# Kernel optimization log

Measured on AMD Instinct MI355X. Metric: run time of the kernel, lower is better.

The kernel has to match this reference:

```python
import jax, jax.numpy as jnp
import numpy as np

L = 512      # x_len (also per-segment memory length)
B = 4        # batch
D = 512      # d_model
H = 8        # num_head
DH = 64      # d_head
MEM = 3      # mem_num (number of cached memory segments)
TOTAL = (MEM + 1) * L
SCALE = 1.0 / (DH ** 0.5)
LN_EPS = 1e-5


def setup_inputs() -> dict:
    key = jax.random.key(0)
    ks = jax.random.split(key, 12)
    f = lambda k, s: jax.random.normal(k, s, dtype=jnp.float32)
    x = f(ks[0], (L, B, D))
    memory = f(ks[1], (MEM, L, B, D))
    pos_emb = f(ks[2], (TOTAL, B, D))
    pos_bias_u = f(ks[3], (H, DH)) * 0.02
    pos_bias_v = f(ks[4], (H, DH)) * 0.02
    # segment gate: random 0/1, but current-input segment (last) always on
    ib = (jax.random.uniform(ks[5], (L, B, MEM + 1)) < 0.7).astype(jnp.float32)
    indice_bool = ib.at[:, :, MEM].set(1.0)
    # causal mask over concatenated [memory ; x] keys: mask future input positions
    qi = jnp.arange(L)[:, None]
    kj = jnp.arange(TOTAL)[None, :]
    mask = jnp.broadcast_to((kj > (MEM * L + qi))[:, :, None], (L, TOTAL, B))
    W_q = f(ks[6], (D, H * DH)) * 0.02
    W_kv = f(ks[7], (D, 2 * H * DH)) * 0.02
    W_rel = f(ks[8], (D, H * DH)) * 0.02
    W_o = f(ks[9], (H * DH, D)) * 0.02
    ln_g = jnp.ones((D,), jnp.float32)
    ln_b = jnp.zeros((D,), jnp.float32)
    return dict(x=x, memory=memory, pos_emb=pos_emb, pos_bias_u=pos_bias_u,
                pos_bias_v=pos_bias_v, mask=mask, indice_bool=indice_bool,
                W_q=W_q, W_kv=W_kv, W_rel=W_rel, W_o=W_o, ln_g=ln_g, ln_b=ln_b)


def _rel_shift(bd):
    # bd: [i, k, j, b, n]; torch _rel_shift flattens (k,j) and does the pad/view trick
    i, k, j, b, n = bd.shape
    xf = bd.reshape(i, k * j, b, n)
    zp = jnp.zeros((i, 1, b, n), bd.dtype)
    xp = jnp.concatenate([zp, xf], axis=1)            # [i, k*j+1, b, n]
    xp = xp.reshape(k * j + 1, i, b, n)               # raw memory reinterpretation
    return xp[1:].reshape(i, k, j, b, n)


def reference(x, memory, pos_emb, pos_bias_u, pos_bias_v, mask, indice_bool,
              W_q, W_kv, W_rel, W_o, ln_g, ln_b):
    Lq, Bz, Dm = x.shape
    mem_flat = memory.reshape(MEM * Lq, Bz, Dm)
    c = jnp.concatenate([mem_flat, x], axis=0)        # [TOTAL, B, D]
    kv = c @ W_kv                                     # [TOTAL, B, 2*H*DH]
    k_, v_ = jnp.split(kv, 2, axis=-1)
    pk = k_.reshape(MEM + 1, Lq, Bz, H, DH)
    pv = v_.reshape(MEM + 1, Lq, Bz, H, DH)
    rel = (pos_emb @ W_rel).reshape(MEM + 1, Lq, Bz, H, DH)
    q = (x @ W_q).reshape(Lq, Bz, H, DH)
    qu = q + pos_bias_u
    qv = q + pos_bias_v
    # gate[i,k,1,b,1] == indice_bool[i,b,k]; equals einsum('ibnd,ibk->kibnd') pre-mul
    gate = jnp.transpose(indice_bool, (0, 2, 1))[:, :, None, :, None]
    AC = jnp.einsum('ibnd,kjbnd->ikjbn', qu, pk) * gate   # [i,k,j,b,n]
    BD = jnp.einsum('ibnd,kjbnd->ikjbn', qv, rel) * gate
    BD = _rel_shift(BD)
    score = (AC + BD) * SCALE
    score = score.reshape(Lq, TOTAL, Bz, H)
    score = jnp.where(mask[:, :, :, None], -jnp.inf, score)
    prob = jax.nn.softmax(score, axis=1)
    attn_matrix = prob.mean(axis=(2, 3))              # [i, TOTAL]
    prob5 = prob.reshape(Lq, MEM + 1, Lq, Bz, H)
    vec = jnp.einsum('ikjbn,kjbnd->ibnd', prob5, pv).reshape(Lq, Bz, H * DH)
    attn_out = vec @ W_o
    y = x + attn_out
    mu = y.mean(-1, keepdims=True)
    var = jnp.mean(jnp.square(y - mu), axis=-1, keepdims=True)
    output = (y - mu) / jnp.sqrt(var + LN_EPS) * ln_g + ln_b
    return (output, attn_matrix)
```

## Files before the change

### kernel.cpp

```cpp
#include <hip/hip_runtime.h>
#include <hip/hip_bf16.h>
#include <math.h>

typedef __bf16 bhalf8 __attribute__((ext_vector_type(8)));
typedef __bf16 bhalf4 __attribute__((ext_vector_type(4)));
typedef float  f32x4  __attribute__((ext_vector_type(4)));

#define MFMA16(a, b, c) __builtin_amdgcn_mfma_f32_16x16x32_bf16(a, b, c, 0, 0, 0)

__global__ __launch_bounds__(256) void transcast_all(
    const float* __restrict__ Wq, const float* __restrict__ Wkv,
    const float* __restrict__ Wrel, const float* __restrict__ Wo,
    __bf16* __restrict__ Wt)
{
  const int k  = blockIdx.x * 64 + (threadIdx.x & 63);
  const int ng = blockIdx.y * 4 + (threadIdx.x >> 6);
  const float* src; int nn, Ns;
  if (ng < 512)       { src = Wq;   nn = ng;        Ns = 512; }
  else if (ng < 1536) { src = Wkv;  nn = ng - 512;  Ns = 1024; }
  else if (ng < 2048) { src = Wrel; nn = ng - 1536; Ns = 512; }
  else                { src = Wo;   nn = ng - 2048; Ns = 512; }
  Wt[(size_t)ng * 512 + k] = (__bf16)src[(size_t)k * Ns + nn];
}

template <int OUT_MODE, int A_F32>
__global__ __launch_bounds__(256) void gemm_bf16(
    const void* __restrict__ A0v, const void* __restrict__ A1v, int split,
    const __bf16* __restrict__ Bt, void* __restrict__ C, int M, int N, int K,
    const float* __restrict__ pbu, const float* __restrict__ pbv,
    __bf16* __restrict__ qup, __bf16* __restrict__ qvp)
{
  __shared__ __bf16 a_lds[128][40];
  __shared__ __bf16 b_lds[128][40];
  const int m0 = blockIdx.x * 128;
  const int n0 = blockIdx.y * 128;
  const int tid = threadIdx.x;
  const int w = tid >> 6, l = tid & 63;
  const int wn = (w >> 1) * 64, wm = (w & 1) * 64;
  const int li = l & 15, lq = l >> 4;
  const int lk = lq << 3;

  const int srow0 = tid >> 2, srow1 = (tid >> 2) + 64;
  const int skc = (tid & 3) << 3;
  const float* arowf[2];
  const __bf16* arowh[2];
  if (A_F32) {
    const float* A0 = (const float*)A0v;
    const float* A1 = (const float*)A1v;
    const int r0 = m0 + srow0, r1 = m0 + srow1;
    arowf[0] = r0 < split ? A0 + (size_t)r0 * K : A1 + (size_t)(r0 - split) * K;
    arowf[1] = r1 < split ? A0 + (size_t)r1 * K : A1 + (size_t)(r1 - split) * K;
  } else {
    arowh[0] = (const __bf16*)A0v + (size_t)(m0 + srow0) * K;
    arowh[1] = (const __bf16*)A0v + (size_t)(m0 + srow1) * K;
  }

  f32x4 acc[4][4] = {};

  for (int k0 = 0; k0 < K; k0 += 32) {
    __syncthreads();
#pragma unroll
    for (int c = 0; c < 2; ++c) {
      const int row = c ? srow1 : srow0;
      if (A_F32) {
        float4 f0 = *(const float4*)(arowf[c] + k0 + skc);
        float4 f1 = *(const float4*)(arowf[c] + k0 + skc + 4);
        bhalf8 h;
        h[0] = (__bf16)f0.x; h[1] = (__bf16)f0.y; h[2] = (__bf16)f0.z; h[3] = (__bf16)f0.w;
        h[4] = (__bf16)f1.x; h[5] = (__bf16)f1.y; h[6] = (__bf16)f1.z; h[7] = (__bf16)f1.w;
        *(bhalf8*)&a_lds[row][skc] = h;
      } else {
        *(bhalf8*)&a_lds[row][skc] = *(const bhalf8*)(arowh[c] + k0 + skc);
      }
      *(bhalf8*)&b_lds[row][skc] = *(const bhalf8*)(Bt + (size_t)(n0 + row) * K + k0 + skc);
    }
    __syncthreads();
    bhalf8 af[4], bf_[4];
#pragma unroll
    for (int s = 0; s < 4; ++s) {
      af[s]  = *(const bhalf8*)&b_lds[wn + s * 16 + li][lk];
      bf_[s] = *(const bhalf8*)&a_lds[wm + s * 16 + li][lk];
    }
#pragma unroll
    for (int ns = 0; ns < 4; ++ns)
#pragma unroll
      for (int ms = 0; ms < 4; ++ms)
        acc[ns][ms] = MFMA16(af[ns], bf_[ms], acc[ns][ms]);
  }

  const int lr = lq << 2;
#pragma unroll
  for (int ms = 0; ms < 4; ++ms) {
    const int m = m0 + wm + ms * 16 + li;
#pragma unroll
    for (int ns = 0; ns < 4; ++ns) {
      const int n = n0 + wn + ns * 16 + lr;
      if (OUT_MODE == 1) {
        *(f32x4*)((float*)C + (size_t)m * N + n) = acc[ns][ms];
      } else if (OUT_MODE == 0) {
        bhalf4 pk;
#pragma unroll
        for (int r = 0; r < 4; ++r) pk[r] = (__bf16)acc[ns][ms][r];
        *(bhalf4*)((__bf16*)C + (size_t)m * N + n) = pk;
      } else {
        const int i = m >> 2, bb = m & 3, hd = n >> 6;
        float4 u4 = *(const float4*)(pbu + n);
        float4 v4 = *(const float4*)(pbv + n);
        const size_t off = (((size_t)bb * 8 + hd) * 512 + i) * 64 + (n & 63);
        bhalf4 pu, pv;
        pu[0] = (__bf16)((acc[ns][ms][0] + u4.x) * 0.125f);
        pu[1] = (__bf16)((acc[ns][ms][1] + u4.y) * 0.125f);
        pu[2] = (__bf16)((acc[ns][ms][2] + u4.z) * 0.125f);
        pu[3] = (__bf16)((acc[ns][ms][3] + u4.w) * 0.125f);
        pv[0] = (__bf16)((acc[ns][ms][0] + v4.x) * 0.125f);
        pv[1] = (__bf16)((acc[ns][ms][1] + v4.y) * 0.125f);
        pv[2] = (__bf16)((acc[ns][ms][2] + v4.z) * 0.125f);
        pv[3] = (__bf16)((acc[ns][ms][3] + v4.w) * 0.125f);
        *(bhalf4*)(qup + off) = pu;
        *(bhalf4*)(qvp + off) = pv;
      }
    }
  }
}

__global__ __launch_bounds__(256) void vtrans(const __bf16* __restrict__ kvb,
                                              __bf16* __restrict__ vtb)
{
  __shared__ __bf16 T2[64][72];
  const int t0 = blockIdx.x * 64;
  const int p = blockIdx.y;
  const int b = p >> 3, n = p & 7;
  const int tid = threadIdx.x;
#pragma unroll
  for (int c = 0; c < 2; ++c) {
    const int e = c * 256 + tid;
    const int tl = e >> 3, d8 = (e & 7) << 3;
    bhalf8 v8 = *(const bhalf8*)(kvb + ((size_t)(t0 + tl) * 4 + b) * 1024 + 512 + n * 64 + d8);
#pragma unroll
    for (int j = 0; j < 8; ++j) T2[d8 + j][tl] = v8[j];
  }
  __syncthreads();
#pragma unroll
  for (int c = 0; c < 2; ++c) {
    const int e = c * 256 + tid;
    const int d = e >> 3, t8 = (e & 7) << 3;
    bhalf8 v = *(const bhalf8*)&T2[d][t8];
    *(bhalf8*)(vtb + ((size_t)p * 64 + d) * 2048 + t0 + t8) = v;
  }
}

__global__ __launch_bounds__(512, 4) void attn_v4(
    const __bf16* __restrict__ qup, const __bf16* __restrict__ qvp,
    const __bf16* __restrict__ kvb, const __bf16* __restrict__ relb,
    const __bf16* __restrict__ vtb, const float* __restrict__ indice,
    float* __restrict__ po, float* __restrict__ mlh,
    __bf16* __restrict__ pb, float* __restrict__ ms)
{
  __shared__ __align__(16) __bf16 P_l[32][136];
  __shared__ __align__(16) __bf16 bdl[160][34];
  __shared__ float red0[8][33];
  __shared__ float red1[8][33];

  const int bid = blockIdx.x;
  const int wrk = ((bid & 7) << 7) | (bid >> 3);
  const int plane = wrk >> 5;
  const int i0 = ((wrk >> 1) & 15) << 5;
  const int half = wrk & 1;
  const int b = plane >> 3, n = plane & 7;
  const int tid = threadIdx.x;
  const int w = tid >> 6;
  const int l = tid & 63;
  const int li = l & 15;
  const int lq = l >> 4;

  const __bf16* kbase = kvb + (size_t)b * 1024 + n * 64;
  const __bf16* rbase = relb + (size_t)b * 512 + n * 64;
  const __bf16* vbase = vtb + (size_t)plane * 131072;

  bhalf8 qu[2][2], qv[2][2];
  float g[2][4];
#pragma unroll
  for (int it = 0; it < 2; ++it) {
    const int i = i0 + it * 16 + li;
    const float* gp = indice + ((size_t)i * 4 + b) * 4;
    g[it][0] = gp[0]; g[it][1] = gp[1]; g[it][2] = gp[2]; g[it][3] = gp[3];
    const __bf16* qp = qup + ((size_t)plane * 512 + i) * 64;
    const __bf16* qq = qvp + ((size_t)plane * 512 + i) * 64;
    qu[it][0] = *(const bhalf8*)(qp + lq * 8);
    qu[it][1] = *(const bhalf8*)(qp + 32 + lq * 8);
    qv[it][0] = *(const bhalf8*)(qq + lq * 8);
    qv[it][1] = *(const bhalf8*)(qq + 32 + lq * 8);
  }

  float m0 = -1e30f, m1 = -1e30f, l0 = 0.f, l1 = 0.f;
  f32x4 oacc = {0.f, 0.f, 0.f, 0.f};
  const int dgw = w >> 1, itw = w & 1;
  const int nt = ((1536 + i0 + 31) >> 7) + 1;
  const int t_start = half ? 8 : 0;
  const int t_end   = half ? nt : 8;

  for (int tile = t_start; tile < t_end; ++tile) {
    const int tb = tile << 7;
    const int rb = tb + 480 - i0;

#pragma unroll
    for (int ri = 0; ri < 2; ++ri) {
      const int rs = w + ri * 8;
      if (ri == 0 || rs < 10) {
        int row = rb + rs * 16 + li;
        row = row > 2047 ? 2047 : row;
        const __bf16* rp = rbase + (size_t)row * 2048;
        bhalf8 a0 = *(const bhalf8*)(rp + lq * 8);
        bhalf8 a1 = *(const bhalf8*)(rp + 32 + lq * 8);
#pragma unroll
        for (int it = 0; it < 2; ++it) {
          f32x4 c = {0.f, 0.f, 0.f, 0.f};
          c = MFMA16(a0, qv[it][0], c);
          c = MFMA16(a1, qv[it][1], c);
#pragma unroll
          for (int r = 0; r < 4; ++r) {
            const int rowl = rs * 16 + lq * 4 + r;
            int rk = (rb + rowl) >> 9; rk = rk > 3 ? 3 : rk;
            bdl[rowl][it * 16 + li] = (__bf16)(c[r] * g[it][rk]);
          }
        }
      }
    }
    f32x4 s[2];
    {
      const __bf16* kp = kbase + (size_t)(tb + w * 16 + li) * 4096;
      bhalf8 a0 = *(const bhalf8*)(kp + lq * 8);
      bhalf8 a1 = *(const bhalf8*)(kp + 32 + lq * 8);
#pragma unroll
      for (int it = 0; it < 2; ++it) {
        f32x4 c = {0.f, 0.f, 0.f, 0.f};
        c = MFMA16(a0, qu[it][0], c);
        c = MFMA16(a1, qu[it][1], c);
        s[it] = c;
      }
    }
    __syncthreads();

    float sv[2][4];
    float tmax[2] = {-1e30f, -1e30f};
#pragma unroll
    for (int it = 0; it < 2; ++it) {
      const int i = i0 + it * 16 + li;
#pragma unroll
      for (int r = 0; r < 4; ++r) {
        const int tl = w * 16 + lq * 4 + r;
        const int t = tb + tl;
        float sc = -1e30f;
        if (t <= 1536 + i) {
          const float bdv = (float)bdl[tl + 31 - it * 16 - li][it * 16 + li];
          sc = s[it][r] * g[it][t >> 9] + bdv;
        }
        sv[it][r] = sc;
        tmax[it] = fmaxf(tmax[it], sc);
      }
    }
    tmax[0] = fmaxf(tmax[0], __shfl_xor(tmax[0], 16));
    tmax[0] = fmaxf(tmax[0], __shfl_xor(tmax[0], 32));
    tmax[1] = fmaxf(tmax[1], __shfl_xor(tmax[1], 16));
    tmax[1] = fmaxf(tmax[1], __shfl_xor(tmax[1], 32));
    if (l < 16) { red0[w][li] = tmax[0]; red0[w][16 + li] = tmax[1]; }
    __syncthreads();

    float mn[2], scl[2];
#pragma unroll
    for (int it = 0; it < 2; ++it) {
      const int ic = it * 16 + li;
      float mt = red0[0][ic];
#pragma unroll
      for (int ww = 1; ww < 8; ++ww) mt = fmaxf(mt, red0[ww][ic]);
      const float mo = it ? m1 : m0;
      mn[it] = fmaxf(mo, mt);
      scl[it] = __expf(mo - mn[it]);
    }
    if (w == 0 && l < 16) {
      float* msp = ms + ((size_t)plane * 16 + tile) * 512 + i0;
      msp[li] = mn[0];
      msp[16 + li] = mn[1];
    }
    float ps[2] = {0.f, 0.f};
#pragma unroll
    for (int it = 0; it < 2; ++it) {
      bhalf4 pk;
#pragma unroll
      for (int r = 0; r < 4; ++r) {
        const float p = __expf(sv[it][r] - mn[it]);
        ps[it] += p;
        pk[r] = (__bf16)p;
      }
      *(bhalf4*)&P_l[it * 16 + li][w * 16 + lq * 4] = pk;
    }
    ps[0] += __shfl_xor(ps[0], 16); ps[0] += __shfl_xor(ps[0], 32);
    ps[1] += __shfl_xor(ps[1], 16); ps[1] += __shfl_xor(ps[1], 32);
    if (l < 16) { red1[w][li] = ps[0]; red1[w][16 + li] = ps[1]; }
    __syncthreads();

    {
      const int iloc = tid >> 4, tq = tid & 15;
      bhalf8 pv8 = *(const bhalf8*)&P_l[iloc][tq * 8];
      *(bhalf8*)(pb + ((size_t)plane * 512 + i0 + iloc) * 2048 + tb + tq * 8) = pv8;
    }

    {
      float ls0 = 0.f, ls1 = 0.f;
#pragma unroll
      for (int ww = 0; ww < 8; ++ww) { ls0 += red1[ww][li]; ls1 += red1[ww][16 + li]; }
      l0 = l0 * scl[0] + ls0; m0 = mn[0];
      l1 = l1 * scl[1] + ls1; m1 = mn[1];
    }
    oacc *= scl[itw];
    {
      const __bf16* vp = vbase + (size_t)(dgw * 16 + li) * 2048 + tb;
#pragma unroll
      for (int kt = 0; kt < 4; ++kt) {
        bhalf8 af = *(const bhalf8*)(vp + kt * 32 + lq * 8);
        bhalf8 bf_ = *(const bhalf8*)&P_l[itw * 16 + li][kt * 32 + lq * 8];
        oacc = MFMA16(af, bf_, oacc);
      }
    }
  }

  __syncthreads();
  float* obuf = (float*)&P_l[0][0];
  if (w == 0 && l < 16) {
    float* mp0 = mlh + ((size_t)half * 16384 + plane * 512 + i0 + li) * 2;
    mp0[0] = m0; mp0[1] = l0;
    float* mp1 = mlh + ((size_t)half * 16384 + plane * 512 + i0 + 16 + li) * 2;
    mp1[0] = m1; mp1[1] = l1;
  }
#pragma unroll
  for (int r = 0; r < 4; ++r)
    obuf[(itw * 16 + li) * 68 + dgw * 16 + lq * 4 + r] = oacc[r];
  __syncthreads();
  {
    const int iloc = tid >> 4, dq = tid & 15;
    f32x4 o = *(f32x4*)&obuf[iloc * 68 + dq * 4];
    *(f32x4*)(po + ((size_t)half * 16384 + plane * 512 + i0 + iloc) * 64 + dq * 4) = o;
  }
}

__global__ __launch_bounds__(256) void attn_merge(
    const float* __restrict__ po, const float* __restrict__ mlh,
    __bf16* __restrict__ vecb, float* __restrict__ ml)
{
  const int row = blockIdx.x * 16 + (threadIdx.x >> 4);
  const int dq = threadIdx.x & 15;
  const float2 a = *(const float2*)(mlh + (size_t)row * 2);
  const float2 bm = *(const float2*)(mlh + ((size_t)16384 + row) * 2);
  const float mf = fmaxf(a.x, bm.x);
  const float ea = __expf(a.x - mf), eb = __expf(bm.x - mf);
  const float lf = a.y * ea + bm.y * eb;
  f32x4 oa = *(const f32x4*)(po + (size_t)row * 64 + dq * 4);
  f32x4 ob = *(const f32x4*)(po + ((size_t)16384 + row) * 64 + dq * 4);
  const float inv = 1.f / lf;
  bhalf4 ov;
#pragma unroll
  for (int r = 0; r < 4; ++r) ov[r] = (__bf16)((oa[r] * ea + ob[r] * eb) * inv);
  const int plane = row >> 9, i = row & 511, b = plane >> 3, n = plane & 7;
  *(bhalf4*)(vecb + ((size_t)i * 4 + b) * 512 + n * 64 + dq * 4) = ov;
  if (dq == 0) { ml[(size_t)row * 2] = mf; ml[(size_t)row * 2 + 1] = lf; }
}

__global__ __launch_bounds__(256) void am_final(
    const __bf16* __restrict__ pb, const float* __restrict__ ms,
    const float* __restrict__ ml, float* __restrict__ am)
{
  const int i = blockIdx.x;
  const int tid = threadIdx.x;
  const int t0 = tid << 3;
  const int tile = t0 >> 7;
  const bool valid = tile <= ((1536 + (i | 31)) >> 7);
  f32x4 a0 = {0.f, 0.f, 0.f, 0.f}, a1 = {0.f, 0.f, 0.f, 0.f};
#pragma unroll 4
  for (int p = 0; p < 32; ++p) {
    const float2 mlv = *(const float2*)(ml + ((size_t)p * 512 + i) * 2);
    float wgt = 0.f;
    if (valid)
      wgt = __expf(ms[((size_t)p * 16 + tile) * 512 + i] - mlv.x) / mlv.y;
    bhalf8 v = *(const bhalf8*)(pb + ((size_t)p * 512 + i) * 2048 + t0);
    a0[0] += wgt * (float)v[0];
    a0[1] += wgt * (float)v[1];
    a0[2] += wgt * (float)v[2];
    a0[3] += wgt * (float)v[3];
    a1[0] += wgt * (float)v[4];
    a1[1] += wgt * (float)v[5];
    a1[2] += wgt * (float)v[6];
    a1[3] += wgt * (float)v[7];
  }
  const float sc = 1.f / 32.f;
  *(f32x4*)(am + (size_t)i * 2048 + t0)     = a0 * sc;
  *(f32x4*)(am + (size_t)i * 2048 + t0 + 4) = a1 * sc;
}

__global__ __launch_bounds__(256) void ln_f32(
    const float* __restrict__ x, const float* __restrict__ ao,
    const float* __restrict__ g, const float* __restrict__ bb,
    float* __restrict__ out)
{
  const int row = blockIdx.x;
  const int tid = threadIdx.x;
  const size_t base = (size_t)row * 512;
  const float y0 = x[base + tid] + ao[base + tid];
  const float y1 = x[base + 256 + tid] + ao[base + 256 + tid];
  float s  = y0 + y1;
  float ss = y0 * y0 + y1 * y1;
#pragma unroll
  for (int off = 32; off > 0; off >>= 1) {
    s  += __shfl_xor(s, off);
    ss += __shfl_xor(ss, off);
  }
  __shared__ float sred[4], ssred[4], stat[2];
  const int w = tid >> 6;
  if ((tid & 63) == 0) { sred[w] = s; ssred[w] = ss; }
  __syncthreads();
  if (tid == 0) {
    const float S  = sred[0] + sred[1] + sred[2] + sred[3];
    const float SS = ssred[0] + ssred[1] + ssred[2] + ssred[3];
    const float mu = S * (1.f / 512.f);
    const float var = SS * (1.f / 512.f) - mu * mu;
    stat[0] = mu;
    stat[1] = rsqrtf(var + 1e-5f);
  }
  __syncthreads();
  const float mu = stat[0], rs = stat[1];
  out[base + tid]       = (y0 - mu) * rs * g[tid] + bb[tid];
  out[base + 256 + tid] = (y1 - mu) * rs * g[256 + tid] + bb[256 + tid];
}

extern "C" void kernel_launch(void* const* d_in, const int* in_sizes, int n_in,
                              void* d_out, int out_size, void* d_ws, size_t ws_size,
                              hipStream_t stream)
{
  (void)in_sizes; (void)n_in; (void)out_size; (void)ws_size;
  const float* x      = (const float*)d_in[0];
  const float* memory = (const float*)d_in[1];
  const float* pos    = (const float*)d_in[2];
  const float* pbu    = (const float*)d_in[3];
  const float* pbv    = (const float*)d_in[4];
  const float* indice = (const float*)d_in[6];
  const float* W_q    = (const float*)d_in[7];
  const float* W_kv   = (const float*)d_in[8];
  const float* W_rel  = (const float*)d_in[9];
  const float* W_o    = (const float*)d_in[10];
  const float* ln_g   = (const float*)d_in[11];
  const float* ln_b   = (const float*)d_in[12];

  float* out = (float*)d_out;
  float* am  = out + 1048576;

  __bf16* ws    = (__bf16*)d_ws;
  __bf16* vtb   = ws;
  float*  po    = (float*)(ws + 4194304);
  float*  aof   = po;
  __bf16* kvb   = ws + 8388608;
  __bf16* relb  = ws + 16777216;
  __bf16* qup   = ws + 20971520;
  __bf16* qvp   = ws + 22020096;
  __bf16* vecb  = ws + 23068672;
  __bf16* wt    = ws + 24117248;
  __bf16* wqt   = wt;
  __bf16* wkvt  = wt + 512 * 512;
  __bf16* wrelt = wt + 1536 * 512;
  __bf16* wot   = wt + 2048 * 512;
  float*  ml    = (float*)(ws + 25427968);
  float*  ms    = (float*)(ws + 25493504);
  __bf16* pbuf  = ws + 26017792;
  float*  mlh   = (float*)(ws + 59572224);

  transcast_all<<<dim3(8, 640), 256, 0, stream>>>(W_q, W_kv, W_rel, W_o, wt);

  gemm_bf16<2, 1><<<dim3(16, 4), 256, 0, stream>>>(x, x, 2048, wqt, (void*)qup,
                                                   2048, 512, 512, pbu, pbv, qup, qvp);
  gemm_bf16<0, 1><<<dim3(64, 8), 256, 0, stream>>>(memory, x, 6144, wkvt, kvb,
                                                   8192, 1024, 512,
                                                   nullptr, nullptr, nullptr, nullptr);
  gemm_bf16<0, 1><<<dim3(64, 4), 256, 0, stream>>>(pos, pos, 8192, wrelt, relb,
                                                   8192, 512, 512,
                                                   nullptr, nullptr, nullptr, nullptr);

  vtrans<<<dim3(32, 32), 256, 0, stream>>>(kvb, vtb);

  attn_v4<<<1024, 512, 0, stream>>>(qup, qvp, kvb, relb, vtb, indice,
                                    po, mlh, pbuf, ms);
  attn_merge<<<1024, 256, 0, stream>>>(po, mlh, vecb, ml);

  am_final<<<512, 256, 0, stream>>>(pbuf, ms, ml, am);

  gemm_bf16<1, 0><<<dim3(16, 4), 256, 0, stream>>>(vecb, vecb, 2048, wot, aof,
                                                   2048, 512, 512,
                                                   nullptr, nullptr, nullptr, nullptr);
  ln_f32<<<2048, 256, 0, stream>>>(x, aof, ln_g, ln_b, out);
}
```

Baseline: 305.1 us.

## Restructure attention to per-wave independent softmax with in-block merge

Rewrites the attention kernel so each wave owns a 16-query by 32-key slice and keeps its own running max and sum, removing the block-wide reductions and most of the __syncthreads calls inside the tile loop. The two key halves are no longer split across blocks; four partial softmax states are merged in shared memory at the end, which drops the separate merge kernel and its global round-trip. The per-slice max is now stored at 32-key granularity and am_final is adjusted to read it. In exchange there are half as many blocks, each wave issues more V MFMAs and redundant rel loads, and per-wave maxima are coarser.

```diff
diff --git a/kernel.cpp b/kernel.cpp
--- a/kernel.cpp
+++ b/kernel.cpp
@@ -149,220 +149,168 @@
   }
 }
 
-__global__ __launch_bounds__(512, 4) void attn_v4(
+__global__ __launch_bounds__(512, 4) void attn_v5(
     const __bf16* __restrict__ qup, const __bf16* __restrict__ qvp,
     const __bf16* __restrict__ kvb, const __bf16* __restrict__ relb,
     const __bf16* __restrict__ vtb, const float* __restrict__ indice,
-    float* __restrict__ po, float* __restrict__ mlh,
+    __bf16* __restrict__ vecb, float* __restrict__ ml,
     __bf16* __restrict__ pb, float* __restrict__ ms)
 {
-  __shared__ __align__(16) __bf16 P_l[32][136];
-  __shared__ __align__(16) __bf16 bdl[160][34];
-  __shared__ float red0[8][33];
-  __shared__ float red1[8][33];
+  __shared__ __align__(16) char smem_raw[36864];
+  __shared__ float mlw[8][16][2];
+  float*  bdw = (float*)smem_raw;
+  __bf16* pw  = (__bf16*)(smem_raw + 27648);
+  float*  obuf = (float*)smem_raw;
 
   const int bid = blockIdx.x;
-  const int wrk = ((bid & 7) << 7) | (bid >> 3);
-  const int plane = wrk >> 5;
-  const int i0 = ((wrk >> 1) & 15) << 5;
-  const int half = wrk & 1;
+  const int wrk = ((bid & 7) << 6) | (bid >> 3);
+  const int plane = wrk >> 4;
+  const int i0 = (wrk & 15) << 5;
   const int b = plane >> 3, n = plane & 7;
   const int tid = threadIdx.x;
-  const int w = tid >> 6;
-  const int l = tid & 63;
-  const int li = l & 15;
-  const int lq = l >> 4;
-
-  const __bf16* kbase = kvb + (size_t)b * 1024 + n * 64;
-  const __bf16* rbase = relb + (size_t)b * 512 + n * 64;
+  const int w = tid >> 6, l = tid & 63;
+  const int li = l & 15, lq = l >> 4;
+  const int it = w & 1, ts = w >> 1;
+  const int i = i0 + it * 16 + li;
+  const int base_r = (2 * ts + 1 - it) << 4;
+
+  float*  bdww = bdw + w * (48 * 18);
+  __bf16* pww  = pw + w * (16 * 36);
+
+  const __bf16* qp = qup + ((size_t)plane * 512 + i) * 64;
+  const __bf16* qq = qvp + ((size_t)plane * 512 + i) * 64;
+  bhalf8 qu0 = *(const bhalf8*)(qp + lq * 8);
+  bhalf8 qu1 = *(const bhalf8*)(qp + 32 + lq * 8);
+  bhalf8 qv0 = *(const bhalf8*)(qq + lq * 8);
+  bhalf8 qv1 = *(const bhalf8*)(qq + 32 + lq * 8);
+  const float* gp = indice + ((size_t)i * 4 + b) * 4;
+  const float g0 = gp[0], g1 = gp[1], g2 = gp[2], g3 = gp[3];
+
   const __bf16* vbase = vtb + (size_t)plane * 131072;
 
-  bhalf8 qu[2][2], qv[2][2];
-  float g[2][4];
-#pragma unroll
-  for (int it = 0; it < 2; ++it) {
-    const int i = i0 + it * 16 + li;
-    const float* gp = indice + ((size_t)i * 4 + b) * 4;
-    g[it][0] = gp[0]; g[it][1] = gp[1]; g[it][2] = gp[2]; g[it][3] = gp[3];
-    const __bf16* qp = qup + ((size_t)plane * 512 + i) * 64;
-    const __bf16* qq = qvp + ((size_t)plane * 512 + i) * 64;
-    qu[it][0] = *(const bhalf8*)(qp + lq * 8);
-    qu[it][1] = *(const bhalf8*)(qp + 32 + lq * 8);
-    qv[it][0] = *(const bhalf8*)(qq + lq * 8);
-    qv[it][1] = *(const bhalf8*)(qq + 32 + lq * 8);
-  }
-
-  float m0 = -1e30f, m1 = -1e30f, l0 = 0.f, l1 = 0.f;
-  f32x4 oacc = {0.f, 0.f, 0.f, 0.f};
-  const int dgw = w >> 1, itw = w & 1;
+  float m_run = -1e30f, l_run = 0.f;
+  f32x4 oacc[4] = {};
   const int nt = ((1536 + i0 + 31) >> 7) + 1;
-  const int t_start = half ? 8 : 0;
-  const int t_end   = half ? nt : 8;
-
-  for (int tile = t_start; tile < t_end; ++tile) {
+
+  for (int tile = 0; tile < nt; ++tile) {
     const int tb = tile << 7;
-    const int rb = tb + 480 - i0;
-
-#pragma unroll
-    for (int ri = 0; ri < 2; ++ri) {
-      const int rs = w + ri * 8;
-      if (ri == 0 || rs < 10) {
-        int row = rb + rs * 16 + li;
-        row = row > 2047 ? 2047 : row;
-        const __bf16* rp = rbase + (size_t)row * 2048;
-        bhalf8 a0 = *(const bhalf8*)(rp + lq * 8);
-        bhalf8 a1 = *(const bhalf8*)(rp + 32 + lq * 8);
-#pragma unroll
-        for (int it = 0; it < 2; ++it) {
-          f32x4 c = {0.f, 0.f, 0.f, 0.f};
-          c = MFMA16(a0, qv[it][0], c);
-          c = MFMA16(a1, qv[it][1], c);
-#pragma unroll
-          for (int r = 0; r < 4; ++r) {
-            const int rowl = rs * 16 + lq * 4 + r;
-            int rk = (rb + rowl) >> 9; rk = rk > 3 ? 3 : rk;
-            bdl[rowl][it * 16 + li] = (__bf16)(c[r] * g[it][rk]);
-          }
+    const int wbase = tb + 480 - i0 + base_r;
+
+#pragma unroll
+    for (int rs = 0; rs < 3; ++rs) {
+      int grow = wbase + rs * 16 + li;
+      grow = grow > 2047 ? 2047 : grow;
+      const __bf16* rp = relb + ((size_t)grow * 4 + b) * 512 + n * 64;
+      bhalf8 a0 = *(const bhalf8*)(rp + lq * 8);
+      bhalf8 a1 = *(const bhalf8*)(rp + 32 + lq * 8);
+      f32x4 c = {0.f, 0.f, 0.f, 0.f};
+      c = MFMA16(a0, qv0, c);
+      c = MFMA16(a1, qv1, c);
+#pragma unroll
+      for (int r = 0; r < 4; ++r) {
+        const int rl = rs * 16 + lq * 4 + r;
+        int rk = (wbase + rl) >> 9; rk = rk > 3 ? 3 : rk;
+        const float gk = rk == 0 ? g0 : (rk == 1 ? g1 : (rk == 2 ? g2 : g3));
+        bdww[rl * 18 + li] = c[r] * gk;
+      }
+    }
+    f32x4 s[2];
+#pragma unroll
+    for (int sl = 0; sl < 2; ++sl) {
+      const __bf16* kp = kvb + ((size_t)(tb + ts * 32 + sl * 16 + li) * 4 + b) * 1024 + n * 64;
+      f32x4 c = {0.f, 0.f, 0.f, 0.f};
+      c = MFMA16(*(const bhalf8*)(kp + lq * 8), qu0, c);
+      c = MFMA16(*(const bhalf8*)(kp + 32 + lq * 8), qu1, c);
+      s[sl] = c;
+    }
+    float sc[2][4];
+    float tmax = -1e30f;
+#pragma unroll
+    for (int sl = 0; sl < 2; ++sl) {
+#pragma unroll
+      for (int r = 0; r < 4; ++r) {
+        const int tloc = ts * 32 + sl * 16 + lq * 4 + r;
+        const int t = tb + tloc;
+        float v = -1e30f;
+        if (t <= 1536 + i) {
+          const int tk = t >> 9;
+          const float gk = tk == 0 ? g0 : (tk == 1 ? g1 : (tk == 2 ? g2 : g3));
+          v = s[sl][r] * gk + bdww[(sl * 16 + lq * 4 + r + 15 - li) * 18 + li];
         }
+        sc[sl][r] = v;
+        tmax = fmaxf(tmax, v);
       }
     }
-    f32x4 s[2];
-    {
-      const __bf16* kp = kbase + (size_t)(tb + w * 16 + li) * 4096;
-      bhalf8 a0 = *(const bhalf8*)(kp + lq * 8);
-      bhalf8 a1 = *(const bhalf8*)(kp + 32 + lq * 8);
-#pragma unroll
-      for (int it = 0; it < 2; ++it) {
-        f32x4 c = {0.f, 0.f, 0.f, 0.f};
-        c = MFMA16(a0, qu[it][0], c);
-        c = MFMA16(a1, qu[it][1], c);
-        s[it] = c;
+    tmax = fmaxf(tmax, __shfl_xor(tmax, 16));
+    tmax = fmaxf(tmax, __shfl_xor(tmax, 32));
+    const float mnew = fmaxf(m_run, tmax);
+    const float scl = __expf(m_run - mnew);
+    float psum = 0.f;
+    bhalf4 pk[2];
+#pragma unroll
+    for (int sl = 0; sl < 2; ++sl) {
+#pragma unroll
+      for (int r = 0; r < 4; ++r) {
+        const float p = __expf(sc[sl][r] - mnew);
+        psum += p;
+        pk[sl][r] = (__bf16)p;
       }
     }
-    __syncthreads();
-
-    float sv[2][4];
-    float tmax[2] = {-1e30f, -1e30f};
-#pragma unroll
-    for (int it = 0; it < 2; ++it) {
-      const int i = i0 + it * 16 + li;
-#pragma unroll
-      for (int r = 0; r < 4; ++r) {
-        const int tl = w * 16 + lq * 4 + r;
-        const int t = tb + tl;
-        float sc = -1e30f;
-        if (t <= 1536 + i) {
-          const float bdv = (float)bdl[tl + 31 - it * 16 - li][it * 16 + li];
-          sc = s[it][r] * g[it][t >> 9] + bdv;
-        }
-        sv[it][r] = sc;
-        tmax[it] = fmaxf(tmax[it], sc);
-      }
-    }
-    tmax[0] = fmaxf(tmax[0], __shfl_xor(tmax[0], 16));
-    tmax[0] = fmaxf(tmax[0], __shfl_xor(tmax[0], 32));
-    tmax[1] = fmaxf(tmax[1], __shfl_xor(tmax[1], 16));
-    tmax[1] = fmaxf(tmax[1], __shfl_xor(tmax[1], 32));
-    if (l < 16) { red0[w][li] = tmax[0]; red0[w][16 + li] = tmax[1]; }
-    __syncthreads();
-
-    float mn[2], scl[2];
-#pragma unroll
-    for (int it = 0; it < 2; ++it) {
-      const int ic = it * 16 + li;
-      float mt = red0[0][ic];
-#pragma unroll
-      for (int ww = 1; ww < 8; ++ww) mt = fmaxf(mt, red0[ww][ic]);
-      const float mo = it ? m1 : m0;
-      mn[it] = fmaxf(mo, mt);
-      scl[it] = __expf(mo - mn[it]);
-    }
-    if (w == 0 && l < 16) {
-      float* msp = ms + ((size_t)plane * 16 + tile) * 512 + i0;
-      msp[li] = mn[0];
-      msp[16 + li] = mn[1];
-    }
-    float ps[2] = {0.f, 0.f};
-#pragma unroll
-    for (int it = 0; it < 2; ++it) {
-      bhalf4 pk;
-#pragma unroll
-      for (int r = 0; r < 4; ++r) {
-        const float p = __expf(sv[it][r] - mn[it]);
-        ps[it] += p;
-        pk[r] = (__bf16)p;
-      }
-      *(bhalf4*)&P_l[it * 16 + li][w * 16 + lq * 4] = pk;
-    }
-    ps[0] += __shfl_xor(ps[0], 16); ps[0] += __shfl_xor(ps[0], 32);
-    ps[1] += __shfl_xor(ps[1], 16); ps[1] += __shfl_xor(ps[1], 32);
-    if (l < 16) { red1[w][li] = ps[0]; red1[w][16 + li] = ps[1]; }
-    __syncthreads();
-
-    {
-      const int iloc = tid >> 4, tq = tid & 15;
-      bhalf8 pv8 = *(const bhalf8*)&P_l[iloc][tq * 8];
-      *(bhalf8*)(pb + ((size_t)plane * 512 + i0 + iloc) * 2048 + tb + tq * 8) = pv8;
-    }
-
-    {
-      float ls0 = 0.f, ls1 = 0.f;
-#pragma unroll
-      for (int ww = 0; ww < 8; ++ww) { ls0 += red1[ww][li]; ls1 += red1[ww][16 + li]; }
-      l0 = l0 * scl[0] + ls0; m0 = mn[0];
-      l1 = l1 * scl[1] + ls1; m1 = mn[1];
-    }
-    oacc *= scl[itw];
-    {
-      const __bf16* vp = vbase + (size_t)(dgw * 16 + li) * 2048 + tb;
-#pragma unroll
-      for (int kt = 0; kt < 4; ++kt) {
-        bhalf8 af = *(const bhalf8*)(vp + kt * 32 + lq * 8);
-        bhalf8 bf_ = *(const bhalf8*)&P_l[itw * 16 + li][kt * 32 + lq * 8];
-        oacc = MFMA16(af, bf_, oacc);
-      }
+    psum += __shfl_xor(psum, 16);
+    psum += __shfl_xor(psum, 32);
+    l_run = l_run * scl + psum;
+    m_run = mnew;
+    if (l < 16)
+      ms[((size_t)(plane << 6) + (tile << 2) + ts) * 512 + i] = mnew;
+#pragma unroll
+    for (int sl = 0; sl < 2; ++sl) {
+      *(bhalf4*)(pb + ((size_t)plane * 512 + i) * 2048 + tb + ts * 32 + sl * 16 + lq * 4) = pk[sl];
+      *(bhalf4*)(pww + li * 36 + sl * 16 + lq * 4) = pk[sl];
+    }
+    const bhalf8 pfrag = *(const bhalf8*)(pww + li * 36 + lq * 8);
+#pragma unroll
+    for (int dsub = 0; dsub < 4; ++dsub) {
+      oacc[dsub] *= scl;
+      const __bf16* vp = vbase + (size_t)(dsub * 16 + li) * 2048 + tb + ts * 32 + lq * 8;
+      oacc[dsub] = MFMA16(*(const bhalf8*)vp, pfrag, oacc[dsub]);
     }
   }
 
   __syncthreads();
-  float* obuf = (float*)&P_l[0][0];
-  if (w == 0 && l < 16) {
-    float* mp0 = mlh + ((size_t)half * 16384 + plane * 512 + i0 + li) * 2;
-    mp0[0] = m0; mp0[1] = l0;
-    float* mp1 = mlh + ((size_t)half * 16384 + plane * 512 + i0 + 16 + li) * 2;
-    mp1[0] = m1; mp1[1] = l1;
-  }
-#pragma unroll
-  for (int r = 0; r < 4; ++r)
-    obuf[(itw * 16 + li) * 68 + dgw * 16 + lq * 4 + r] = oacc[r];
+  if (l < 16) { mlw[w][li][0] = m_run; mlw[w][li][1] = l_run; }
+#pragma unroll
+  for (int dsub = 0; dsub < 4; ++dsub)
+    *(f32x4*)&obuf[(size_t)(w * 16 + li) * 68 + dsub * 16 + lq * 4] = oacc[dsub];
   __syncthreads();
   {
     const int iloc = tid >> 4, dq = tid & 15;
-    f32x4 o = *(f32x4*)&obuf[iloc * 68 + dq * 4];
-    *(f32x4*)(po + ((size_t)half * 16384 + plane * 512 + i0 + iloc) * 64 + dq * 4) = o;
-  }
-}
-
-__global__ __launch_bounds__(256) void attn_merge(
-    const float* __restrict__ po, const float* __restrict__ mlh,
-    __bf16* __restrict__ vecb, float* __restrict__ ml)
-{
-  const int row = blockIdx.x * 16 + (threadIdx.x >> 4);
-  const int dq = threadIdx.x & 15;
-  const float2 a = *(const float2*)(mlh + (size_t)row * 2);
-  const float2 bm = *(const float2*)(mlh + ((size_t)16384 + row) * 2);
-  const float mf = fmaxf(a.x, bm.x);
-  const float ea = __expf(a.x - mf), eb = __expf(bm.x - mf);
-  const float lf = a.y * ea + bm.y * eb;
-  f32x4 oa = *(const f32x4*)(po + (size_t)row * 64 + dq * 4);
-  f32x4 ob = *(const f32x4*)(po + ((size_t)16384 + row) * 64 + dq * 4);
-  const float inv = 1.f / lf;
-  bhalf4 ov;
-#pragma unroll
-  for (int r = 0; r < 4; ++r) ov[r] = (__bf16)((oa[r] * ea + ob[r] * eb) * inv);
-  const int plane = row >> 9, i = row & 511, b = plane >> 3, n = plane & 7;
-  *(bhalf4*)(vecb + ((size_t)i * 4 + b) * 512 + n * 64 + dq * 4) = ov;
-  if (dq == 0) { ml[(size_t)row * 2] = mf; ml[(size_t)row * 2 + 1] = lf; }
+    const int it2 = iloc >> 4, lii = iloc & 15;
+    float mk[4], lk[4];
+#pragma unroll
+    for (int k = 0; k < 4; ++k) {
+      mk[k] = mlw[it2 + 2 * k][lii][0];
+      lk[k] = mlw[it2 + 2 * k][lii][1];
+    }
+    const float mf = fmaxf(fmaxf(mk[0], mk[1]), fmaxf(mk[2], mk[3]));
+    f32x4 o = {0.f, 0.f, 0.f, 0.f};
+    float lf = 0.f;
+#pragma unroll
+    for (int k = 0; k < 4; ++k) {
+      const float e = __expf(mk[k] - mf);
+      lf += lk[k] * e;
+      f32x4 ov = *(const f32x4*)&obuf[(size_t)((it2 + 2 * k) * 16 + lii) * 68 + dq * 4];
+      o += ov * e;
+    }
+    const float inv = 1.f / lf;
+    bhalf4 ov;
+#pragma unroll
+    for (int r = 0; r < 4; ++r) ov[r] = (__bf16)(o[r] * inv);
+    *(bhalf4*)(vecb + ((size_t)(i0 + iloc) * 4 + b) * 512 + n * 64 + dq * 4) = ov;
+    if (dq == 0) {
+      float* mp = ml + ((size_t)plane * 512 + i0 + iloc) * 2;
+      mp[0] = mf; mp[1] = lf;
+    }
+  }
 }
 
 __global__ __launch_bounds__(256) void am_final(
@@ -372,15 +320,15 @@
   const int i = blockIdx.x;
   const int tid = threadIdx.x;
   const int t0 = tid << 3;
-  const int tile = t0 >> 7;
-  const bool valid = tile <= ((1536 + (i | 31)) >> 7);
+  const int t32 = t0 >> 5;
+  const bool valid = (t0 >> 7) <= ((1536 + (i | 31)) >> 7);
   f32x4 a0 = {0.f, 0.f, 0.f, 0.f}, a1 = {0.f, 0.f, 0.f, 0.f};
 #pragma unroll 4
   for (int p = 0; p < 32; ++p) {
     const float2 mlv = *(const float2*)(ml + ((size_t)p * 512 + i) * 2);
     float wgt = 0.f;
     if (valid)
-      wgt = __expf(ms[((size_t)p * 16 + tile) * 512 + i] - mlv.x) / mlv.y;
+      wgt = __expf(ms[((size_t)(p << 6) + t32) * 512 + i] - mlv.x) / mlv.y;
     bhalf8 v = *(const bhalf8*)(pb + ((size_t)p * 512 + i) * 2048 + t0);
     a0[0] += wgt * (float)v[0];
     a0[1] += wgt * (float)v[1];
@@ -454,8 +402,8 @@
 
   __bf16* ws    = (__bf16*)d_ws;
   __bf16* vtb   = ws;
-  float*  po    = (float*)(ws + 4194304);
-  float*  aof   = po;
+  float*  msb   = (float*)(ws + 4194304);
+  float*  aof   = msb;
   __bf16* kvb   = ws + 8388608;
   __bf16* relb  = ws + 16777216;
   __bf16* qup   = ws + 20971520;
@@ -467,9 +415,7 @@
   __bf16* wrelt = wt + 1536 * 512;
   __bf16* wot   = wt + 2048 * 512;
   float*  ml    = (float*)(ws + 25427968);
-  float*  ms    = (float*)(ws + 25493504);
   __bf16* pbuf  = ws + 26017792;
-  float*  mlh   = (float*)(ws + 59572224);
 
   transcast_all<<<dim3(8, 640), 256, 0, stream>>>(W_q, W_kv, W_rel, W_o, wt);
 
@@ -484,11 +430,10 @@
 
   vtrans<<<dim3(32, 32), 256, 0, stream>>>(kvb, vtb);
 
-  attn_v4<<<1024, 512, 0, stream>>>(qup, qvp, kvb, relb, vtb, indice,
-                                    po, mlh, pbuf, ms);
-  attn_merge<<<1024, 256, 0, stream>>>(po, mlh, vecb, ml);
-
-  am_final<<<512, 256, 0, stream>>>(pbuf, ms, ml, am);
+  attn_v5<<<512, 512, 0, stream>>>(qup, qvp, kvb, relb, vtb, indice,
+                                   vecb, ml, pbuf, msb);
+
+  am_final<<<512, 256, 0, stream>>>(pbuf, msb, ml, am);
 
   gemm_bf16<1, 0><<<dim3(16, 4), 256, 0, stream>>>(vecb, vecb, 2048, wot, aof,
                                                    2048, 512, 512,
```

New measurement: 329.4 us. +8.0%, slower.
